# Performance work log

Measured on AMD Instinct MI355X. Metric: run time of the kernel, lower is better.

## Reference

```python
import jax, jax.numpy as jnp
import numpy as np
import math

D_MODEL = 2048
N_HEADS = 16
HEAD_DIM = D_MODEL // N_HEADS  # 128
SEQ_LEN = 4096
BATCH = 4


def rotate_half(x):
    x1, x2 = x[..., : x.shape[-1] // 2], x[..., x.shape[-1] // 2 :]
    return jnp.concatenate((-x2, x1), axis=-1)


def rope_cos_sin(seq_len, head_dim, dtype=jnp.float32):
    inv_freq = 1.0 / (10000.0 ** (jnp.arange(0, head_dim, 2, dtype=jnp.float32) / head_dim))
    freqs = jnp.arange(seq_len, dtype=jnp.float32)[:, None] * inv_freq[None, :]  # [S, D/2]
    emb = jnp.concatenate((freqs, freqs), axis=-1)  # [S, D]
    return jnp.cos(emb).astype(dtype), jnp.sin(emb).astype(dtype)


def setup_inputs() -> dict:
    key = jax.random.key(0)
    kx, kq, kk, kv = jax.random.split(key, 4)
    x = jax.random.normal(kx, (BATCH, SEQ_LEN, D_MODEL), dtype=jnp.float32)
    s = 1.0 / math.sqrt(D_MODEL)
    # torch Linear weight: [out_features, in_features]
    w_q = jax.random.uniform(kq, (HEAD_DIM, D_MODEL), minval=-s, maxval=s, dtype=jnp.float32)
    w_k = jax.random.uniform(kk, (HEAD_DIM, D_MODEL), minval=-s, maxval=s, dtype=jnp.float32)
    w_v = jax.random.uniform(kv, (HEAD_DIM, D_MODEL), minval=-s, maxval=s, dtype=jnp.float32)
    return {"x": x, "w_q": w_q, "w_k": w_k, "w_v": w_v}


def reference(x, w_q, w_k, w_v):
    B, S, _ = x.shape
    scale = 1.0 / math.sqrt(HEAD_DIM)
    # projections: x @ W^T  -> [B, S, head_dim]
    q = jnp.einsum('bsd,hd->bsh', x, w_q)
    k = jnp.einsum('bsd,hd->bsh', x, w_k)
    v = jnp.einsum('bsd,hd->bsh', x, w_v)
    cos, sin = rope_cos_sin(S, HEAD_DIM, x.dtype)  # [S, head_dim]
    q = q * cos + rotate_half(q) * sin
    k = k * cos + rotate_half(k) * sin
    scores = jnp.einsum('bqh,bkh->bqk', q, k) * scale  # [B, S, S]
    causal = jnp.tril(jnp.ones((S, S), dtype=bool))
    scores = jnp.where(causal[None, :, :], scores, -jnp.inf)
    attn = jax.nn.softmax(scores, axis=-1)
    out = jnp.einsum('bqk,bkh->bqh', attn, v)  # [B, S, head_dim]
    return out
```

## Files before the change

### kernel.cpp

```cpp
#include <hip/hip_runtime.h>
#include <hip/hip_bf16.h>

#define BATCH 4
#define SEQ 4096
#define DMODEL 2048
#define HD 128
#define BS (BATCH*SEQ)

typedef __attribute__((ext_vector_type(8))) short short8;
typedef __attribute__((ext_vector_type(4))) float f32x4;
typedef __attribute__((ext_vector_type(4))) float float4v;
typedef unsigned short u16;
typedef unsigned int u32;

#define LOG2E 1.4426950408889634f
#define SCALE 0.08838834764831845f

__device__ __forceinline__ u16 f2bf(float f){
  u32 u = __builtin_bit_cast(u32, f);
  u32 r = (u + 0x7FFFu + ((u >> 16) & 1u)) >> 16;
  return (u16)r;
}
__device__ __forceinline__ float bf2f(u16 b){
  u32 u = ((u32)b) << 16;
  return __builtin_bit_cast(float, u);
}

__device__ __forceinline__ void gload16(const void* gptr, void* lptr){
  __builtin_amdgcn_global_load_lds((const __attribute__((address_space(1))) void*)gptr,
                                   (__attribute__((address_space(3))) void*)lptr, 16, 0, 0);
}

__global__ __launch_bounds__(256) void k_prep(float2* __restrict__ tab,
                                              const float* __restrict__ wq, const float* __restrict__ wk,
                                              const float* __restrict__ wv, u16* __restrict__ wb){
  int bidx = blockIdx.x;
  if (bidx < 1024){
    int i = bidx*256 + threadIdx.x;
    int s = i >> 6, j = i & 63;
    float invf = (float)pow(10000.0, -(double)j/64.0);
    float ang  = (float)s * invf;
    double a = (double)ang;
    tab[i] = make_float2((float)cos(a), (float)sin(a));
  } else {
    int i = (bidx - 1024)*256 + threadIdx.x;
    int m = i >> 18; int r = i & 262143;
    const float* s = (m==0) ? wq : ((m==1) ? wk : wv);
    wb[i] = f2bf(s[r]);
  }
}

__global__ __launch_bounds__(256) void k_cvtx(const float* __restrict__ x, u16* __restrict__ xb){
  size_t i = (size_t)blockIdx.x*256 + threadIdx.x;
  const float4v* xp = (const float4v*)x;
  float4v a = xp[i*2], c = xp[i*2+1];
  short8 o;
  o[0]=(short)f2bf(a[0]); o[1]=(short)f2bf(a[1]); o[2]=(short)f2bf(a[2]); o[3]=(short)f2bf(a[3]);
  o[4]=(short)f2bf(c[0]); o[5]=(short)f2bf(c[1]); o[6]=(short)f2bf(c[2]); o[7]=(short)f2bf(c[3]);
  *(short8*)(xb + i*8) = o;
}

__global__ __launch_bounds__(256) void k_gemm(
    const u16* __restrict__ xb, const u16* __restrict__ wb, const float2* __restrict__ tab,
    u16* __restrict__ qb, u16* __restrict__ kb, u16* __restrict__ vt)
{
  __shared__ u16 lA[128*64];
  __shared__ u16 lW[128*64];
  const int tid = threadIdx.x;
  const int wsel = blockIdx.y;
  const size_t M0 = (size_t)blockIdx.x * 128;
  const u16* Wm = wb + (size_t)wsel * (HD*DMODEL);
  const int w = tid >> 6, lane = tid & 63, lr = lane & 15, lg = lane >> 4;

  f32x4 acc[2][8];
  #pragma unroll
  for (int i=0;i<2;i++)
    #pragma unroll
    for (int j=0;j<8;j++) acc[i][j] = f32x4{0.f,0.f,0.f,0.f};

  const int Lb = tid*16;
  int srow[4], soff[4];
  #pragma unroll
  for (int i=0;i<4;i++){
    int L = i*4096 + Lb;
    int row = L >> 7, cb = L & 127;
    int scb = cb ^ ((row & 7) << 4);
    srow[i] = row; soff[i] = scb >> 1;
  }

  for (int k0 = 0; k0 < DMODEL; k0 += 64){
    #pragma unroll
    for (int i=0;i<4;i++){
      gload16(xb + (M0 + srow[i])*DMODEL + k0 + soff[i], ((char*)lA) + i*4096 + Lb);
      gload16(Wm + (size_t)srow[i]*DMODEL + k0 + soff[i], ((char*)lW) + i*4096 + Lb);
    }
    __syncthreads();
    short8 afr[2][2], bfr[8][2];
    #pragma unroll
    for (int rf=0; rf<2; rf++)
      #pragma unroll
      for (int ks=0; ks<2; ks++){
        int r = w*32 + rf*16 + lr;
        int byte = r*128 + ((ks*64 + lg*16) ^ ((r&7)<<4));
        afr[rf][ks] = *(const short8*)((const char*)lA + byte);
      }
    #pragma unroll
    for (int nf=0; nf<8; nf++)
      #pragma unroll
      for (int ks=0; ks<2; ks++){
        int r = nf*16 + lr;
        int byte = r*128 + ((ks*64 + lg*16) ^ ((r&7)<<4));
        bfr[nf][ks] = *(const short8*)((const char*)lW + byte);
      }
    #pragma unroll
    for (int rf=0; rf<2; rf++)
      #pragma unroll
      for (int nf=0; nf<8; nf++){
        acc[rf][nf] = __builtin_amdgcn_mfma_f32_16x16x32_bf16(afr[rf][0], bfr[nf][0], acc[rf][nf], 0,0,0);
        acc[rf][nf] = __builtin_amdgcn_mfma_f32_16x16x32_bf16(afr[rf][1], bfr[nf][1], acc[rf][nf], 0,0,0);
      }
    __syncthreads();
  }

  if (wsel < 2){
    u16* dst = (wsel == 0) ? qb : kb;
    #pragma unroll
    for (int rf=0; rf<2; rf++){
      #pragma unroll
      for (int reg=0; reg<4; reg++){
        size_t grow = M0 + w*32 + rf*16 + lg*4 + reg;
        int spos = (int)(grow & (SEQ-1));
        #pragma unroll
        for (int cf=0; cf<4; cf++){
          int j = cf*16 + lr;
          float2 cs = tab[spos*64 + j];
          float lo = acc[rf][cf][reg];
          float hi = acc[rf][cf+4][reg];
          dst[grow*HD + j]      = f2bf(lo*cs.x - hi*cs.y);
          dst[grow*HD + j + 64] = f2bf(hi*cs.x + lo*cs.y);
        }
      }
    }
  } else {
    #pragma unroll
    for (int rf=0; rf<2; rf++)
      #pragma unroll
      for (int reg=0; reg<4; reg++){
        size_t grow = M0 + w*32 + rf*16 + lg*4 + reg;
        size_t b = grow >> 12;
        size_t spos = grow & (SEQ-1);
        #pragma unroll
        for (int cf=0; cf<8; cf++){
          int col = cf*16 + lr;
          vt[(b*HD + col)*SEQ + spos] = f2bf(acc[rf][cf][reg]);
        }
      }
  }
}

__global__ __launch_bounds__(256) void k_attn(
    const u16* __restrict__ qbuf, const u16* __restrict__ kb, const u16* __restrict__ vt,
    u16* __restrict__ Opart, float2* __restrict__ ml)
{
  __shared__ u16 lK[64*128];
  __shared__ u16 lV[128*64];
  __shared__ u16 lP[4][16*64];
  const int tid = threadIdx.x;
  const int bid = blockIdx.x;
  const int x = bid & 7, idx = bid >> 3;
  const int b = x >> 1, half = x & 1;
  const int qt = 63 - (idx >> 1);
  const int sp = (idx & 1) + 2*half;
  const int qbn = b*64 + qt;
  const int w = tid >> 6, lane = tid & 63, lr = lane & 15, lg = lane >> 4;

  const int n = qt + 1, cbase = n >> 2, crem = n & 3;
  const int cnt = cbase + (sp < crem ? 1 : 0);
  const int klo = sp*cbase + (sp < crem ? sp : crem);
  const int khi = klo + cnt;
  const size_t prow0 = ((size_t)qbn*4 + sp)*64;

  if (cnt == 0){
    if (lr == 0){
      #pragma unroll
      for (int reg=0; reg<4; reg++)
        ml[prow0 + w*16 + lg*4 + reg] = make_float2(-1e30f, 0.f);
    }
    return;
  }

  const size_t qrow = (size_t)b*SEQ + qt*64 + w*16 + lr;
  short8 aq[4];
  #pragma unroll
  for (int ks=0; ks<4; ks++)
    aq[ks] = *(const short8*)(qbuf + qrow*HD + ks*32 + lg*8);

  f32x4 accO[8];
  #pragma unroll
  for (int i=0;i<8;i++) accO[i] = f32x4{0.f,0.f,0.f,0.f};
  float m2[4]   = {-1e30f,-1e30f,-1e30f,-1e30f};
  float lsum[4] = {0.f,0.f,0.f,0.f};

  const int Lb = tid*16;
  const float cfac = SCALE * LOG2E;

  for (int kt = klo; kt < khi; kt++){
    #pragma unroll
    for (int i=0;i<4;i++){
      int L = i*4096 + Lb;
      { int row = L >> 8, cb = L & 255;
        int scb = cb ^ ((row & 7) << 4);
        gload16(kb + ((size_t)b*SEQ + kt*64 + row)*HD + (scb>>1), ((char*)lK) + L); }
      { int row = L >> 7, cb = L & 127;
        int scb = cb ^ ((row & 7) << 4);
        gload16(vt + ((size_t)b*HD + row)*SEQ + kt*64 + (scb>>1), ((char*)lV) + L); }
    }
    __syncthreads();

    f32x4 sc[4];
    #pragma unroll
    for (int nf=0; nf<4; nf++){
      sc[nf] = f32x4{0.f,0.f,0.f,0.f};
      #pragma unroll
      for (int ks=0; ks<4; ks++){
        int r = nf*16 + lr;
        int byte = r*256 + ((ks*64 + lg*16) ^ ((r&7)<<4));
        short8 bk = *(const short8*)((const char*)lK + byte);
        sc[nf] = __builtin_amdgcn_mfma_f32_16x16x32_bf16(aq[ks], bk, sc[nf], 0,0,0);
      }
      sc[nf] *= cfac;
    }
    if (kt == qt){
      #pragma unroll
      for (int nf=0; nf<4; nf++)
        #pragma unroll
        for (int reg=0; reg<4; reg++){
          int col = nf*16 + lr;
          int row = w*16 + lg*4 + reg;
          if (col > row) sc[nf][reg] = -1e30f;
        }
    }
    float al[4];
    #pragma unroll
    for (int reg=0; reg<4; reg++){
      float v = fmaxf(fmaxf(sc[0][reg], sc[1][reg]), fmaxf(sc[2][reg], sc[3][reg]));
      v = fmaxf(v, __shfl_xor(v, 1));
      v = fmaxf(v, __shfl_xor(v, 2));
      v = fmaxf(v, __shfl_xor(v, 4));
      v = fmaxf(v, __shfl_xor(v, 8));
      float mnew = fmaxf(m2[reg], v);
      al[reg] = exp2f(m2[reg] - mnew);
      m2[reg] = mnew;
    }
    float prs[4] = {0.f,0.f,0.f,0.f};
    #pragma unroll
    for (int nf=0; nf<4; nf++)
      #pragma unroll
      for (int reg=0; reg<4; reg++){
        float p = exp2f(sc[nf][reg] - m2[reg]);
        prs[reg] += p;
        int r = lg*4 + reg;
        int byte = r*128 + ((nf*32 + lr*2) ^ ((r&7)<<4));
        *(u16*)(((char*)lP[w]) + byte) = f2bf(p);
      }
    f32x4 alv = f32x4{al[0], al[1], al[2], al[3]};
    #pragma unroll
    for (int reg=0; reg<4; reg++){
      float v = prs[reg];
      v += __shfl_xor(v, 1);
      v += __shfl_xor(v, 2);
      v += __shfl_xor(v, 4);
      v += __shfl_xor(v, 8);
      lsum[reg] = lsum[reg]*al[reg] + v;
    }
    #pragma unroll
    for (int cf=0; cf<8; cf++) accO[cf] *= alv;

    short8 pa[2];
    #pragma unroll
    for (int ks=0; ks<2; ks++){
      int byte = lr*128 + ((ks*64 + lg*16) ^ ((lr&7)<<4));
      pa[ks] = *(const short8*)(((const char*)lP[w]) + byte);
    }
    #pragma unroll
    for (int cf=0; cf<8; cf++){
      #pragma unroll
      for (int ks=0; ks<2; ks++){
        int d = cf*16 + lr;
        int byte = d*128 + ((ks*64 + lg*16) ^ ((d&7)<<4));
        short8 bv = *(const short8*)(((const char*)lV) + byte);
        accO[cf] = __builtin_amdgcn_mfma_f32_16x16x32_bf16(pa[ks], bv, accO[cf], 0,0,0);
      }
    }
    __syncthreads();
  }

  #pragma unroll
  for (int reg=0; reg<4; reg++){
    size_t pr = prow0 + w*16 + lg*4 + reg;
    #pragma unroll
    for (int cf=0; cf<8; cf++)
      Opart[pr*HD + cf*16 + lr] = f2bf(accO[cf][reg]);
  }
  if (lr == 0){
    #pragma unroll
    for (int reg=0; reg<4; reg++)
      ml[prow0 + w*16 + lg*4 + reg] = make_float2(m2[reg], lsum[reg]);
  }
}

__global__ __launch_bounds__(256) void k_comb(
    const u16* __restrict__ Opart, const float2* __restrict__ ml, float* __restrict__ out)
{
  const int t = threadIdx.x;
  const int r = blockIdx.x*16 + (t >> 4);
  const int c0 = (t & 15)*8;
  const int qbn = r >> 6, rr = r & 63;
  float m[4], l[4], M = -1e30f;
  #pragma unroll
  for (int s=0; s<4; s++){
    float2 v = ml[((size_t)qbn*4 + s)*64 + rr];
    m[s] = v.x; l[s] = v.y;
    M = fmaxf(M, m[s]);
  }
  float L = 0.f;
  #pragma unroll
  for (int s=0; s<4; s++){ m[s] = exp2f(m[s] - M); L += l[s]*m[s]; }
  const float inv = 1.0f / L;
  float acc[8] = {0,0,0,0,0,0,0,0};
  #pragma unroll
  for (int s=0; s<4; s++){
    short8 o = *(const short8*)(Opart + (((size_t)qbn*4 + s)*64 + rr)*(size_t)HD + c0);
    float sc = m[s]*inv;
    #pragma unroll
    for (int j=0;j<8;j++) acc[j] += bf2f((u16)o[j]) * sc;
  }
  f32x4 o0 = f32x4{acc[0],acc[1],acc[2],acc[3]};
  f32x4 o1 = f32x4{acc[4],acc[5],acc[6],acc[7]};
  *(f32x4*)(out + (size_t)r*HD + c0)     = o0;
  *(f32x4*)(out + (size_t)r*HD + c0 + 4) = o1;
}

extern "C" void kernel_launch(void* const* d_in, const int* in_sizes, int n_in,
                              void* d_out, int out_size, void* d_ws, size_t ws_size,
                              hipStream_t stream){
  const float* x  = (const float*)d_in[0];
  const float* wq = (const float*)d_in[1];
  const float* wk = (const float*)d_in[2];
  const float* wv = (const float*)d_in[3];
  float* out = (float*)d_out;
  char* ws = (char*)d_ws;

  size_t off = 0;
  u16* xb = (u16*)(ws + off); off += (size_t)BS*DMODEL*2;
  u16* wb = (u16*)(ws + off); off += (size_t)3*HD*DMODEL*2;
  float2* tab = (float2*)(ws + off); off += (size_t)SEQ*64*8;
  u16* qb = (u16*)(ws + off); off += (size_t)BS*HD*2;
  u16* kb = (u16*)(ws + off); off += (size_t)BS*HD*2;
  u16* vt = (u16*)(ws + off); off += (size_t)BS*HD*2;
  u16* Opart = (u16*)(ws + off); off += (size_t)1024*64*HD*2;
  float2* ml = (float2*)(ws + off); off += (size_t)1024*64*8;
  if (ws_size < off) return;

  hipLaunchKernelGGL(k_prep, dim3(4096),   dim3(256), 0, stream, tab, wq, wk, wv, wb);
  hipLaunchKernelGGL(k_cvtx, dim3(16384),  dim3(256), 0, stream, x, xb);
  hipLaunchKernelGGL(k_gemm, dim3(128,3),  dim3(256), 0, stream, xb, wb, tab, qb, kb, vt);
  hipLaunchKernelGGL(k_attn, dim3(1024),   dim3(256), 0, stream, qb, kb, vt, Opart, ml);
  hipLaunchKernelGGL(k_comb, dim3(1024),   dim3(256), 0, stream, Opart, ml, out);
}
```

Measured before the change: 133.7 us.

## Halve GEMM M-tile to 64 rows and reorder grid so weights share blocks

The projection GEMM tile drops from 128 to 64 rows, doubling the grid from 384 to 768 blocks to fill more of the CUs. Each wave now owns a 16-column slice of the weight and all 64 rows, so its lo/hi RoPE halves sit in its own registers. The grid is reordered so blockIdx.x selects Q/K/V, which puts the three blocks sharing an x tile next to each other for L2 reuse. Launch bounds request 3 blocks per SIMD. The cost is more weight reloads per output and fewer MFMAs per LDS load.

Result: no change. 134.4 us (+0.5%).

```diff
diff --git a/kernel.cpp b/kernel.cpp
--- a/kernel.cpp
+++ b/kernel.cpp
@@ -60,64 +60,70 @@
   *(short8*)(xb + i*8) = o;
 }
 
-__global__ __launch_bounds__(256) void k_gemm(
+__global__ __launch_bounds__(256,3) void k_gemm(
     const u16* __restrict__ xb, const u16* __restrict__ wb, const float2* __restrict__ tab,
     u16* __restrict__ qb, u16* __restrict__ kb, u16* __restrict__ vt)
 {
-  __shared__ u16 lA[128*64];
-  __shared__ u16 lW[128*64];
+  __shared__ char lds[24576];
   const int tid = threadIdx.x;
-  const int wsel = blockIdx.y;
-  const size_t M0 = (size_t)blockIdx.x * 128;
+  const int wsel = blockIdx.x;
+  const int mg = blockIdx.y;
+  const size_t M0 = (size_t)mg * 64;
   const u16* Wm = wb + (size_t)wsel * (HD*DMODEL);
   const int w = tid >> 6, lane = tid & 63, lr = lane & 15, lg = lane >> 4;
 
-  f32x4 acc[2][8];
-  #pragma unroll
-  for (int i=0;i<2;i++)
-    #pragma unroll
-    for (int j=0;j<8;j++) acc[i][j] = f32x4{0.f,0.f,0.f,0.f};
+  f32x4 acc[4][2];
+  #pragma unroll
+  for (int i=0;i<4;i++)
+    #pragma unroll
+    for (int j=0;j<2;j++) acc[i][j] = f32x4{0.f,0.f,0.f,0.f};
 
   const int Lb = tid*16;
-  int srow[4], soff[4];
+  int asrow[2], asoff[2];
+  #pragma unroll
+  for (int i=0;i<2;i++){
+    int L = i*4096 + Lb;
+    int row = L >> 7, cb = L & 127;
+    asrow[i] = row; asoff[i] = (cb ^ ((row & 7) << 4)) >> 1;
+  }
+  int wsrow[4], wsoff[4];
   #pragma unroll
   for (int i=0;i<4;i++){
     int L = i*4096 + Lb;
     int row = L >> 7, cb = L & 127;
-    int scb = cb ^ ((row & 7) << 4);
-    srow[i] = row; soff[i] = scb >> 1;
+    wsrow[i] = row; wsoff[i] = (cb ^ ((row & 7) << 4)) >> 1;
   }
 
   for (int k0 = 0; k0 < DMODEL; k0 += 64){
     #pragma unroll
-    for (int i=0;i<4;i++){
-      gload16(xb + (M0 + srow[i])*DMODEL + k0 + soff[i], ((char*)lA) + i*4096 + Lb);
-      gload16(Wm + (size_t)srow[i]*DMODEL + k0 + soff[i], ((char*)lW) + i*4096 + Lb);
-    }
+    for (int i=0;i<2;i++)
+      gload16(xb + (M0 + asrow[i])*DMODEL + k0 + asoff[i], lds + i*4096 + Lb);
+    #pragma unroll
+    for (int i=0;i<4;i++)
+      gload16(Wm + (size_t)wsrow[i]*DMODEL + k0 + wsoff[i], lds + 8192 + i*4096 + Lb);
     __syncthreads();
-    short8 afr[2][2], bfr[8][2];
-    #pragma unroll
-    for (int rf=0; rf<2; rf++)
+
+    short8 af[4][2], wf[2][2];
+    #pragma unroll
+    for (int rf=0; rf<4; rf++)
       #pragma unroll
       for (int ks=0; ks<2; ks++){
-        int r = w*32 + rf*16 + lr;
-        int byte = r*128 + ((ks*64 + lg*16) ^ ((r&7)<<4));
-        afr[rf][ks] = *(const short8*)((const char*)lA + byte);
-      }
-    #pragma unroll
-    for (int nf=0; nf<8; nf++)
+        int r = rf*16 + lr;
+        af[rf][ks] = *(const short8*)(lds + r*128 + ((ks*64 + lg*16) ^ ((r&7)<<4)));
+      }
+    #pragma unroll
+    for (int nf=0; nf<2; nf++)
       #pragma unroll
       for (int ks=0; ks<2; ks++){
-        int r = nf*16 + lr;
-        int byte = r*128 + ((ks*64 + lg*16) ^ ((r&7)<<4));
-        bfr[nf][ks] = *(const short8*)((const char*)lW + byte);
-      }
-    #pragma unroll
-    for (int rf=0; rf<2; rf++)
-      #pragma unroll
-      for (int nf=0; nf<8; nf++){
-        acc[rf][nf] = __builtin_amdgcn_mfma_f32_16x16x32_bf16(afr[rf][0], bfr[nf][0], acc[rf][nf], 0,0,0);
-        acc[rf][nf] = __builtin_amdgcn_mfma_f32_16x16x32_bf16(afr[rf][1], bfr[nf][1], acc[rf][nf], 0,0,0);
+        int r = w*16 + nf*64 + lr;
+        wf[nf][ks] = *(const short8*)(lds + 8192 + r*128 + ((ks*64 + lg*16) ^ ((r&7)<<4)));
+      }
+    #pragma unroll
+    for (int rf=0; rf<4; rf++)
+      #pragma unroll
+      for (int nf=0; nf<2; nf++){
+        acc[rf][nf] = __builtin_amdgcn_mfma_f32_16x16x32_bf16(af[rf][0], wf[nf][0], acc[rf][nf], 0,0,0);
+        acc[rf][nf] = __builtin_amdgcn_mfma_f32_16x16x32_bf16(af[rf][1], wf[nf][1], acc[rf][nf], 0,0,0);
       }
     __syncthreads();
   }
@@ -125,34 +131,31 @@
   if (wsel < 2){
     u16* dst = (wsel == 0) ? qb : kb;
     #pragma unroll
-    for (int rf=0; rf<2; rf++){
+    for (int rf=0; rf<4; rf++){
       #pragma unroll
       for (int reg=0; reg<4; reg++){
-        size_t grow = M0 + w*32 + rf*16 + lg*4 + reg;
+        size_t grow = M0 + rf*16 + lg*4 + reg;
         int spos = (int)(grow & (SEQ-1));
-        #pragma unroll
-        for (int cf=0; cf<4; cf++){
-          int j = cf*16 + lr;
-          float2 cs = tab[spos*64 + j];
-          float lo = acc[rf][cf][reg];
-          float hi = acc[rf][cf+4][reg];
-          dst[grow*HD + j]      = f2bf(lo*cs.x - hi*cs.y);
-          dst[grow*HD + j + 64] = f2bf(hi*cs.x + lo*cs.y);
-        }
+        int j = w*16 + lr;
+        float2 cs = tab[spos*64 + j];
+        float lo = acc[rf][0][reg];
+        float hi = acc[rf][1][reg];
+        dst[grow*HD + j]      = f2bf(lo*cs.x - hi*cs.y);
+        dst[grow*HD + j + 64] = f2bf(hi*cs.x + lo*cs.y);
       }
     }
   } else {
     #pragma unroll
-    for (int rf=0; rf<2; rf++)
+    for (int rf=0; rf<4; rf++)
       #pragma unroll
       for (int reg=0; reg<4; reg++){
-        size_t grow = M0 + w*32 + rf*16 + lg*4 + reg;
+        size_t grow = M0 + rf*16 + lg*4 + reg;
         size_t b = grow >> 12;
         size_t spos = grow & (SEQ-1);
         #pragma unroll
-        for (int cf=0; cf<8; cf++){
-          int col = cf*16 + lr;
-          vt[(b*HD + col)*SEQ + spos] = f2bf(acc[rf][cf][reg]);
+        for (int nf=0; nf<2; nf++){
+          int col = w*16 + nf*64 + lr;
+          vt[(b*HD + col)*SEQ + spos] = f2bf(acc[rf][nf][reg]);
         }
       }
   }
@@ -364,7 +367,7 @@
 
   hipLaunchKernelGGL(k_prep, dim3(4096),   dim3(256), 0, stream, tab, wq, wk, wv, wb);
   hipLaunchKernelGGL(k_cvtx, dim3(16384),  dim3(256), 0, stream, x, xb);
-  hipLaunchKernelGGL(k_gemm, dim3(128,3),  dim3(256), 0, stream, xb, wb, tab, qb, kb, vt);
+  hipLaunchKernelGGL(k_gemm, dim3(3,256),  dim3(256), 0, stream, xb, wb, tab, qb, kb, vt);
   hipLaunchKernelGGL(k_attn, dim3(1024),   dim3(256), 0, stream, qb, kb, vt, Opart, ml);
   hipLaunchKernelGGL(k_comb, dim3(1024),   dim3(256), 0, stream, Opart, ml, out);
 }
```

## Fuse fp32-to-bf16 x conversion into projection GEMM with single-wave blocks

Applied to the files above, without the earlier changes.

Removes the separate x conversion kernel and its bf16 workspace buffer. The projection GEMM now reads fp32 x directly from global memory, converts it to bf16 in registers, and loads weights straight from global memory without LDS staging. Each block is one wave covering 32 rows times one of the three projections, giving 1536 blocks. This drops a full write and re-read of the converted activation, but each row of x is now read and converted three times, once per projection. The loads are also unstaged and less coalesced, so the GEMM may become latency bound.

Result: slower. 201.3 us (+50.5%).

```diff
diff --git a/kernel.cpp b/kernel.cpp
--- a/kernel.cpp
+++ b/kernel.cpp
@@ -50,27 +50,22 @@
   }
 }
 
-__global__ __launch_bounds__(256) void k_cvtx(const float* __restrict__ x, u16* __restrict__ xb){
-  size_t i = (size_t)blockIdx.x*256 + threadIdx.x;
-  const float4v* xp = (const float4v*)x;
-  float4v a = xp[i*2], c = xp[i*2+1];
-  short8 o;
-  o[0]=(short)f2bf(a[0]); o[1]=(short)f2bf(a[1]); o[2]=(short)f2bf(a[2]); o[3]=(short)f2bf(a[3]);
-  o[4]=(short)f2bf(c[0]); o[5]=(short)f2bf(c[1]); o[6]=(short)f2bf(c[2]); o[7]=(short)f2bf(c[3]);
-  *(short8*)(xb + i*8) = o;
-}
-
-__global__ __launch_bounds__(256) void k_gemm(
-    const u16* __restrict__ xb, const u16* __restrict__ wb, const float2* __restrict__ tab,
+__global__ __launch_bounds__(64) void k_gemm(
+    const float* __restrict__ x, const u16* __restrict__ wb, const float2* __restrict__ tab,
     u16* __restrict__ qb, u16* __restrict__ kb, u16* __restrict__ vt)
 {
-  __shared__ u16 lA[128*64];
-  __shared__ u16 lW[128*64];
-  const int tid = threadIdx.x;
-  const int wsel = blockIdx.y;
-  const size_t M0 = (size_t)blockIdx.x * 128;
+  const int lane = threadIdx.x & 63, lr = lane & 15, lg = lane >> 4;
+  const int bid = blockIdx.x;
+  const int wsel = bid % 3;
+  const int mg = bid / 3;
+  const size_t M0 = (size_t)mg * 32;
   const u16* Wm = wb + (size_t)wsel * (HD*DMODEL);
-  const int w = tid >> 6, lane = tid & 63, lr = lane & 15, lg = lane >> 4;
+
+  const float* ax0 = x + (M0 + lr)*DMODEL + lg*8;
+  const float* ax1 = x + (M0 + 16 + lr)*DMODEL + lg*8;
+  const u16* wp[8];
+  #pragma unroll
+  for (int nf=0; nf<8; nf++) wp[nf] = Wm + (size_t)(nf*16 + lr)*DMODEL + lg*8;
 
   f32x4 acc[2][8];
   #pragma unroll
@@ -78,48 +73,32 @@
     #pragma unroll
     for (int j=0;j<8;j++) acc[i][j] = f32x4{0.f,0.f,0.f,0.f};
 
-  const int Lb = tid*16;
-  int srow[4], soff[4];
-  #pragma unroll
-  for (int i=0;i<4;i++){
-    int L = i*4096 + Lb;
-    int row = L >> 7, cb = L & 127;
-    int scb = cb ^ ((row & 7) << 4);
-    srow[i] = row; soff[i] = scb >> 1;
-  }
-
-  for (int k0 = 0; k0 < DMODEL; k0 += 64){
-    #pragma unroll
-    for (int i=0;i<4;i++){
-      gload16(xb + (M0 + srow[i])*DMODEL + k0 + soff[i], ((char*)lA) + i*4096 + Lb);
-      gload16(Wm + (size_t)srow[i]*DMODEL + k0 + soff[i], ((char*)lW) + i*4096 + Lb);
-    }
-    __syncthreads();
-    short8 afr[2][2], bfr[8][2];
-    #pragma unroll
-    for (int rf=0; rf<2; rf++)
+  for (int t=0; t<32; t++){
+    const int k0 = t*64;
+    short8 af[2][2];
+    #pragma unroll
+    for (int rf=0; rf<2; rf++){
+      const float* ap = (rf == 0) ? ax0 : ax1;
       #pragma unroll
       for (int ks=0; ks<2; ks++){
-        int r = w*32 + rf*16 + lr;
-        int byte = r*128 + ((ks*64 + lg*16) ^ ((r&7)<<4));
-        afr[rf][ks] = *(const short8*)((const char*)lA + byte);
-      }
-    #pragma unroll
-    for (int nf=0; nf<8; nf++)
-      #pragma unroll
-      for (int ks=0; ks<2; ks++){
-        int r = nf*16 + lr;
-        int byte = r*128 + ((ks*64 + lg*16) ^ ((r&7)<<4));
-        bfr[nf][ks] = *(const short8*)((const char*)lW + byte);
-      }
-    #pragma unroll
-    for (int rf=0; rf<2; rf++)
-      #pragma unroll
-      for (int nf=0; nf<8; nf++){
-        acc[rf][nf] = __builtin_amdgcn_mfma_f32_16x16x32_bf16(afr[rf][0], bfr[nf][0], acc[rf][nf], 0,0,0);
-        acc[rf][nf] = __builtin_amdgcn_mfma_f32_16x16x32_bf16(afr[rf][1], bfr[nf][1], acc[rf][nf], 0,0,0);
-      }
-    __syncthreads();
+        float4v a0 = *(const float4v*)(ap + k0 + ks*32);
+        float4v a1 = *(const float4v*)(ap + k0 + ks*32 + 4);
+        short8 o;
+        o[0]=(short)f2bf(a0[0]); o[1]=(short)f2bf(a0[1]); o[2]=(short)f2bf(a0[2]); o[3]=(short)f2bf(a0[3]);
+        o[4]=(short)f2bf(a1[0]); o[5]=(short)f2bf(a1[1]); o[6]=(short)f2bf(a1[2]); o[7]=(short)f2bf(a1[3]);
+        af[rf][ks] = o;
+      }
+    }
+    #pragma unroll
+    for (int nf=0; nf<8; nf++){
+      short8 w0 = *(const short8*)(wp[nf] + k0);
+      short8 w1 = *(const short8*)(wp[nf] + k0 + 32);
+      #pragma unroll
+      for (int rf=0; rf<2; rf++){
+        acc[rf][nf] = __builtin_amdgcn_mfma_f32_16x16x32_bf16(af[rf][0], w0, acc[rf][nf], 0,0,0);
+        acc[rf][nf] = __builtin_amdgcn_mfma_f32_16x16x32_bf16(af[rf][1], w1, acc[rf][nf], 0,0,0);
+      }
+    }
   }
 
   if (wsel < 2){
@@ -128,7 +107,7 @@
     for (int rf=0; rf<2; rf++){
       #pragma unroll
       for (int reg=0; reg<4; reg++){
-        size_t grow = M0 + w*32 + rf*16 + lg*4 + reg;
+        size_t grow = M0 + rf*16 + lg*4 + reg;
         int spos = (int)(grow & (SEQ-1));
         #pragma unroll
         for (int cf=0; cf<4; cf++){
@@ -146,7 +125,7 @@
     for (int rf=0; rf<2; rf++)
       #pragma unroll
       for (int reg=0; reg<4; reg++){
-        size_t grow = M0 + w*32 + rf*16 + lg*4 + reg;
+        size_t grow = M0 + rf*16 + lg*4 + reg;
         size_t b = grow >> 12;
         size_t spos = grow & (SEQ-1);
         #pragma unroll
@@ -352,7 +331,6 @@
   char* ws = (char*)d_ws;
 
   size_t off = 0;
-  u16* xb = (u16*)(ws + off); off += (size_t)BS*DMODEL*2;
   u16* wb = (u16*)(ws + off); off += (size_t)3*HD*DMODEL*2;
   float2* tab = (float2*)(ws + off); off += (size_t)SEQ*64*8;
   u16* qb = (u16*)(ws + off); off += (size_t)BS*HD*2;
@@ -362,9 +340,8 @@
   float2* ml = (float2*)(ws + off); off += (size_t)1024*64*8;
   if (ws_size < off) return;
 
-  hipLaunchKernelGGL(k_prep, dim3(4096),   dim3(256), 0, stream, tab, wq, wk, wv, wb);
-  hipLaunchKernelGGL(k_cvtx, dim3(16384),  dim3(256), 0, stream, x, xb);
-  hipLaunchKernelGGL(k_gemm, dim3(128,3),  dim3(256), 0, stream, xb, wb, tab, qb, kb, vt);
-  hipLaunchKernelGGL(k_attn, dim3(1024),   dim3(256), 0, stream, qb, kb, vt, Opart, ml);
-  hipLaunchKernelGGL(k_comb, dim3(1024),   dim3(256), 0, stream, Opart, ml, out);
-}
+  hipLaunchKernelGGL(k_prep, dim3(4096),  dim3(256), 0, stream, tab, wq, wk, wv, wb);
+  hipLaunchKernelGGL(k_gemm, dim3(1536),  dim3(64),  0, stream, x, wb, tab, qb, kb, vt);
+  hipLaunchKernelGGL(k_attn, dim3(1024),  dim3(256), 0, stream, qb, kb, vt, Opart, ml);
+  hipLaunchKernelGGL(k_comb, dim3(1024),  dim3(256), 0, stream, Opart, ml, out);
+}
```
